# Kernel optimization log

Measured on AMD Instinct MI355X. Metric: run time of the kernel, lower is better.

The kernel has to match this reference:

```python
import jax, jax.numpy as jnp
import numpy as np

KERNEL_SIZE = 5
NUM_BUCKETS = 25


def setup_inputs() -> dict:
    key = jax.random.key(0)
    k1, k2, k3 = jax.random.split(key, 3)
    B, C, H, W = 8, 96, 192, 192
    inp = jax.random.normal(k1, (B, C, H, W), dtype=jnp.float32)
    kernel_bank = jax.random.normal(k2, (NUM_BUCKETS, KERNEL_SIZE, KERNEL_SIZE), dtype=jnp.float32)
    buckets = jax.random.randint(k3, (B, H, W), 0, NUM_BUCKETS, dtype=jnp.int64)
    return {"input": inp, "kernel_bank": kernel_bank, "buckets": buckets}


def reference(input, kernel_bank, buckets):
    # Per-pixel kernel selection from a bank, applied depthwise (same kernel for
    # every channel at a given spatial location), with 'same' zero padding.
    K = KERNEL_SIZE
    p = (K - 1) // 2
    B, C, H, W = input.shape
    xpad = jnp.pad(input, ((0, 0), (0, 0), (p, p), (p, p)))  # [B,C,H+K-1,W+K-1]
    kb = kernel_bank[buckets]  # [B,H,W,K,K] gathered per-pixel kernels
    out = jnp.zeros_like(input)
    # Fixed small loop over the K*K kernel taps (unrolled by jit); avoids
    # materializing a [B,C,H,W,K,K] patch tensor.
    for i in range(K):
        for j in range(K):
            out = out + xpad[:, :, i:i + H, j:j + W] * kb[:, None, :, :, i, j]
    return out
```

## Files before the change

### kernel.cpp

```cpp
#include <hip/hip_runtime.h>


#define KS 5
#define NB 25
#define HALO 2
#define TH 8
#define RPT 2
#define CPG 3
#define WID 192
#define HEI 192
#define CH 96
#define NBATCH 8
#define LPAD 4
#define LROW (LPAD + WID + LPAD)
#define LH (TH + 2 * HALO)
#define CSPLIT 4
#define CPB (CH / CSPLIT)
#define NTHREADS (WID * (TH / RPT))
#define HW ((size_t)HEI * WID)

static_assert(CPB % CPG == 0, "phase count integral");
static_assert(NTHREADS <= 1024, "block size limit");

__device__ __forceinline__ void async16(void* lds, const void* g) {
    __builtin_amdgcn_global_load_lds(
        (const __attribute__((address_space(1))) void*)g,
        (__attribute__((address_space(3))) void*)lds, 16, 0, 0);
}

#define WDECL(R)                                                              \
    float w##R##_0, w##R##_1, w##R##_2, w##R##_3, w##R##_4, w##R##_5,         \
        w##R##_6, w##R##_7, w##R##_8, w##R##_9, w##R##_10, w##R##_11,         \
        w##R##_12, w##R##_13, w##R##_14, w##R##_15, w##R##_16, w##R##_17,     \
        w##R##_18, w##R##_19, w##R##_20, w##R##_21, w##R##_22, w##R##_23,     \
        w##R##_24;

#define WGATH(R)                                                              \
    {                                                                         \
        const float* wp = &sb[bkt##R * (KS * KS)];                            \
        w##R##_0 = wp[0];   w##R##_1 = wp[1];   w##R##_2 = wp[2];             \
        w##R##_3 = wp[3];   w##R##_4 = wp[4];   w##R##_5 = wp[5];             \
        w##R##_6 = wp[6];   w##R##_7 = wp[7];   w##R##_8 = wp[8];             \
        w##R##_9 = wp[9];   w##R##_10 = wp[10]; w##R##_11 = wp[11];           \
        w##R##_12 = wp[12]; w##R##_13 = wp[13]; w##R##_14 = wp[14];           \
        w##R##_15 = wp[15]; w##R##_16 = wp[16]; w##R##_17 = wp[17];           \
        w##R##_18 = wp[18]; w##R##_19 = wp[19]; w##R##_20 = wp[20];           \
        w##R##_21 = wp[21]; w##R##_22 = wp[22]; w##R##_23 = wp[23];           \
        w##R##_24 = wp[24];                                                   \
    }

#define F5(R, T0, T1, T2, T3, T4)                                             \
    acc##R += x0 * w##R##_##T0 + x1 * w##R##_##T1 + x2 * w##R##_##T2          \
            + x3 * w##R##_##T3 + x4 * w##R##_##T4;

#define K0(R) F5(R, 0, 1, 2, 3, 4)
#define K1(R) F5(R, 5, 6, 7, 8, 9)
#define K2(R) F5(R, 10, 11, 12, 13, 14)
#define K3(R) F5(R, 15, 16, 17, 18, 19)
#define K4(R) F5(R, 20, 21, 22, 23, 24)

#define LOADX(CUR, SLAB, I)                                                   \
    {                                                                         \
        const float* rp = &sin_[CUR][SLAB][ty2 + (I)][wcol + (LPAD - HALO)];  \
        x0 = rp[0]; x1 = rp[1]; x2 = rp[2]; x3 = rp[3]; x4 = rp[4];           \
    }

__global__ __launch_bounds__(NTHREADS, 2) void csconv_kernel(
    const float* __restrict__ in, const float* __restrict__ bank,
    const int* __restrict__ buckets, float* __restrict__ out)
{
    __shared__ float sb[NB * KS * KS];
    __shared__ __align__(16) float sin_[2][CPG][LH][LROW];

    const int tid  = threadIdx.x;
    const int wcol = tid % WID;
    const int ty   = tid / WID;
    const int lane = tid & 63;
    const int wv   = tid >> 6;
    const int cg   = blockIdx.x;
    const int ht   = blockIdx.y;
    const int b    = blockIdx.z;
    const int h0   = ht * TH;
    const int r0   = h0 + ty * RPT;

    const int c0 = cg * CPB;
    const float* inb  = in  + (size_t)(b * CH + c0) * HW;
    float*       outb = out + (size_t)(b * CH + c0) * HW;

    if (tid < NB * KS * KS) sb[tid] = bank[tid];

    if (tid < 2 * CPG * LH * 8) {
        const int s = tid / (LH * 8), rem = tid % (LH * 8);
        const int r = rem / 8, p = rem % 8;
        const int col = (p < 4) ? p : (WID + p);
        sin_[s / CPG][s % CPG][r][col] = 0.0f;
    }
    if (h0 - HALO < 0) {
        for (int t = tid; t < 2 * CPG * 2 * LROW; t += NTHREADS) {
            const int s = t / (2 * LROW), rem = t % (2 * LROW);
            sin_[s / CPG][s % CPG][rem / LROW][rem % LROW] = 0.0f;
        }
    }
    if (h0 + TH + HALO > HEI) {
        for (int t = tid; t < 2 * CPG * 2 * LROW; t += NTHREADS) {
            const int s = t / (2 * LROW), rem = t % (2 * LROW);
            sin_[s / CPG][s % CPG][LH - 2 + rem / LROW][rem % LROW] = 0.0f;
        }
    }

#pragma unroll
    for (int k = 0; k < CPG; ++k) {
        const int m  = CPG * wv + k;
        const int s  = m / LH;
        const int rr = m % LH;
        const int hg = h0 - HALO + rr;
        if (hg >= 0 && hg < HEI && lane < 48)
            async16(&sin_[0][s][rr][LPAD],
                    inb + (size_t)s * HW + (size_t)hg * WID + lane * 4);
    }

    __syncthreads();

    const int bkt0 = buckets[(b * HEI + r0 + 0) * WID + wcol];
    const int bkt1 = buckets[(b * HEI + r0 + 1) * WID + wcol];
    WDECL(0) WDECL(1)
    WGATH(0) WGATH(1)

    const int ty2 = ty * RPT;

#define CONV_STORE(CUR, SLAB, CIDX)                                           \
    {                                                                         \
        float acc0 = 0.0f, acc1 = 0.0f;                                       \
        float x0, x1, x2, x3, x4;                                             \
        LOADX(CUR, SLAB, 0) K0(0)                                             \
        LOADX(CUR, SLAB, 1) K1(0) K0(1)                                       \
        LOADX(CUR, SLAB, 2) K2(0) K1(1)                                       \
        LOADX(CUR, SLAB, 3) K3(0) K2(1)                                       \
        LOADX(CUR, SLAB, 4) K4(0) K3(1)                                       \
        LOADX(CUR, SLAB, 5) K4(1)                                             \
        float* op = outb + (size_t)(CIDX) * HW + (size_t)r0 * WID + wcol;     \
        op[0 * WID] = acc0; op[1 * WID] = acc1;                               \
    }

    for (int c = 0; c < CPB; c += CPG) {
        const int cur = (c / CPG) & 1;
        const bool has_next = (c + CPG < CPB);

        if (has_next) {
            const int nxt = cur ^ 1;
#pragma unroll
            for (int k = 0; k < CPG; ++k) {
                const int m  = CPG * wv + k;
                const int s  = m / LH;
                const int rr = m % LH;
                const int hg = h0 - HALO + rr;
                if (hg >= 0 && hg < HEI && lane < 48)
                    async16(&sin_[nxt][s][rr][LPAD],
                            inb + (size_t)(c + CPG + s) * HW
                                + (size_t)hg * WID + lane * 4);
            }
        }

        CONV_STORE(cur, 0, c)
        CONV_STORE(cur, 1, c + 1)
        CONV_STORE(cur, 2, c + 2)

        if (has_next) {
            asm volatile("s_waitcnt vmcnt(6)" ::: "memory");
            __builtin_amdgcn_s_barrier();
            asm volatile("" ::: "memory");
        }
    }
}

extern "C" void kernel_launch(void* const* d_in, const int* in_sizes, int n_in,
                              void* d_out, int out_size, void* d_ws, size_t ws_size,
                              hipStream_t stream) {
    const float* in      = (const float*)d_in[0];
    const float* bank    = (const float*)d_in[1];
    const int*   buckets = (const int*)d_in[2];
    float*       out     = (float*)d_out;
    dim3 grid(CSPLIT, HEI / TH, NBATCH);
    csconv_kernel<<<grid, NTHREADS, 0, stream>>>(in, bank, buckets, out);
}
```

Measured before the change: 211.2 us.

## Tile width into 64-column blocks with halo loads and smaller channel groups

Splits the full 192-wide row tile into three 64-column tiles per block, each staging its own halo columns into LDS, and cuts the per-stage channel group from 3 to 2. Blocks shrink from 768 to 256 threads, the grid triples, and launch bounds now ask for 8 blocks per CU, aiming at higher occupancy and better latency hiding. The cost is redundant halo loads at tile edges and narrower, partly unaligned global-to-LDS copies.

```diff
diff --git a/kernel.cpp b/kernel.cpp
--- a/kernel.cpp
+++ b/kernel.cpp
@@ -6,21 +6,21 @@
 #define HALO 2
 #define TH 8
 #define RPT 2
-#define CPG 3
+#define CPG 2
+#define TILE 64
 #define WID 192
 #define HEI 192
 #define CH 96
 #define NBATCH 8
-#define LPAD 4
-#define LROW (LPAD + WID + LPAD)
+#define LROW (TILE + 8)
 #define LH (TH + 2 * HALO)
 #define CSPLIT 4
 #define CPB (CH / CSPLIT)
-#define NTHREADS (WID * (TH / RPT))
+#define NXT (WID / TILE)
+#define NTHREADS (TILE * (TH / RPT))
 #define HW ((size_t)HEI * WID)
 
 static_assert(CPB % CPG == 0, "phase count integral");
-static_assert(NTHREADS <= 1024, "block size limit");
 
 __device__ __forceinline__ void async16(void* lds, const void* g) {
     __builtin_amdgcn_global_load_lds(
@@ -61,72 +61,9 @@
 
 #define LOADX(CUR, SLAB, I)                                                   \
     {                                                                         \
-        const float* rp = &sin_[CUR][SLAB][ty2 + (I)][wcol + (LPAD - HALO)];  \
+        const float* rp = &sin_[CUR][SLAB][ty2 + (I)][xoff];                  \
         x0 = rp[0]; x1 = rp[1]; x2 = rp[2]; x3 = rp[3]; x4 = rp[4];           \
     }
-
-__global__ __launch_bounds__(NTHREADS, 2) void csconv_kernel(
-    const float* __restrict__ in, const float* __restrict__ bank,
-    const int* __restrict__ buckets, float* __restrict__ out)
-{
-    __shared__ float sb[NB * KS * KS];
-    __shared__ __align__(16) float sin_[2][CPG][LH][LROW];
-
-    const int tid  = threadIdx.x;
-    const int wcol = tid % WID;
-    const int ty   = tid / WID;
-    const int lane = tid & 63;
-    const int wv   = tid >> 6;
-    const int cg   = blockIdx.x;
-    const int ht   = blockIdx.y;
-    const int b    = blockIdx.z;
-    const int h0   = ht * TH;
-    const int r0   = h0 + ty * RPT;
-
-    const int c0 = cg * CPB;
-    const float* inb  = in  + (size_t)(b * CH + c0) * HW;
-    float*       outb = out + (size_t)(b * CH + c0) * HW;
-
-    if (tid < NB * KS * KS) sb[tid] = bank[tid];
-
-    if (tid < 2 * CPG * LH * 8) {
-        const int s = tid / (LH * 8), rem = tid % (LH * 8);
-        const int r = rem / 8, p = rem % 8;
-        const int col = (p < 4) ? p : (WID + p);
-        sin_[s / CPG][s % CPG][r][col] = 0.0f;
-    }
-    if (h0 - HALO < 0) {
-        for (int t = tid; t < 2 * CPG * 2 * LROW; t += NTHREADS) {
-            const int s = t / (2 * LROW), rem = t % (2 * LROW);
-            sin_[s / CPG][s % CPG][rem / LROW][rem % LROW] = 0.0f;
-        }
-    }
-    if (h0 + TH + HALO > HEI) {
-        for (int t = tid; t < 2 * CPG * 2 * LROW; t += NTHREADS) {
-            const int s = t / (2 * LROW), rem = t % (2 * LROW);
-            sin_[s / CPG][s % CPG][LH - 2 + rem / LROW][rem % LROW] = 0.0f;
-        }
-    }
-
-#pragma unroll
-    for (int k = 0; k < CPG; ++k) {
-        const int m  = CPG * wv + k;
-        const int s  = m / LH;
-        const int rr = m % LH;
-        const int hg = h0 - HALO + rr;
-        if (hg >= 0 && hg < HEI && lane < 48)
-            async16(&sin_[0][s][rr][LPAD],
-                    inb + (size_t)s * HW + (size_t)hg * WID + lane * 4);
-    }
-
-    __syncthreads();
-
-    const int bkt0 = buckets[(b * HEI + r0 + 0) * WID + wcol];
-    const int bkt1 = buckets[(b * HEI + r0 + 1) * WID + wcol];
-    WDECL(0) WDECL(1)
-    WGATH(0) WGATH(1)
-
-    const int ty2 = ty * RPT;
 
 #define CONV_STORE(CUR, SLAB, CIDX)                                           \
     {                                                                         \
@@ -138,35 +75,103 @@
         LOADX(CUR, SLAB, 3) K3(0) K2(1)                                       \
         LOADX(CUR, SLAB, 4) K4(0) K3(1)                                       \
         LOADX(CUR, SLAB, 5) K4(1)                                             \
-        float* op = outb + (size_t)(CIDX) * HW + (size_t)r0 * WID + wcol;     \
-        op[0 * WID] = acc0; op[1 * WID] = acc1;                               \
+        float* op = outb + (size_t)(CIDX) * HW + (size_t)r0 * WID + gcol;     \
+        op[0] = acc0; op[WID] = acc1;                                         \
     }
+
+#define STAGE(BUF, CBASE)                                                     \
+    _Pragma("unroll")                                                         \
+    for (int k = 0; k < 6; ++k) {                                             \
+        const int m  = 6 * wv + k;                                 \
+        const int s  = m / LH;                                 \
+        const int rr = m % LH;                          \
+        const int hg = h0 - HALO + rr;                                        \
+        if (hg >= 0 && hg < HEI && lane < nl)                                 \
+            async16(&sin_[BUF][s][rr][dst0],                                  \
+                    inb + (size_t)((CBASE) + s) * HW + (size_t)hg * WID       \
+                        + src0 + lane * 4);                                   \
+    }
+
+__global__ __launch_bounds__(NTHREADS, 8) void csconv_kernel(
+    const float* __restrict__ in, const float* __restrict__ bank,
+    const int* __restrict__ buckets, float* __restrict__ out)
+{
+    __shared__ float sb[NB * KS * KS];
+    __shared__ __align__(16) float sin_[2][CPG][LH][LROW];
+
+    const int tid  = threadIdx.x;
+    const int wcol = tid % TILE;
+    const int ty   = tid / TILE;
+    const int lane = tid & 63;
+    const int wv   = tid >> 6;
+    const int bx   = blockIdx.x;
+    const int cx   = bx % NXT;
+    const int cg   = bx / NXT;
+    const int ht   = blockIdx.y;
+    const int b    = blockIdx.z;
+    const int h0   = ht * TH;
+    const int r0   = h0 + ty * RPT;
+    const int gcol = cx * TILE + wcol;
+
+    const int c0 = cg * CPB;
+    const float* inb  = in  + (size_t)(b * CH + c0) * HW;
+    float*       outb = out + (size_t)(b * CH + c0) * HW;
+
+    const int src0 = (cx == 0) ? 0 : (cx * TILE - 4);
+    const int dst0 = (cx == 0) ? 4 : 0;
+    const int nl   = (cx == 1) ? 18 : 17;
+
+    for (int t = tid; t < NB * KS * KS; t += NTHREADS) sb[t] = bank[t];
+
+    if (cx != 1 && tid < 2 * CPG * LH * 4) {
+        const int buf = tid / (CPG * LH * 4);
+        const int s   = (tid / (LH * 4)) % CPG;
+        const int r   = (tid / 4) % LH;
+        const int p   = tid & 3;
+        sin_[buf][s][r][(cx == 0 ? 0 : TILE + 4) + p] = 0.0f;
+    }
+    if (h0 - HALO < 0) {
+        for (int t = tid; t < 2 * CPG * 2 * LROW; t += NTHREADS) {
+            const int buf = t / (CPG * 2 * LROW);
+            const int rem = t % (CPG * 2 * LROW);
+            const int s   = rem / (2 * LROW);
+            const int r   = (rem / LROW) % 2;
+            sin_[buf][s][r][rem % LROW] = 0.0f;
+        }
+    }
+    if (h0 + TH + HALO > HEI) {
+        for (int t = tid; t < 2 * CPG * 2 * LROW; t += NTHREADS) {
+            const int buf = t / (CPG * 2 * LROW);
+            const int rem = t % (CPG * 2 * LROW);
+            const int s   = rem / (2 * LROW);
+            const int r   = (rem / LROW) % 2;
+            sin_[buf][s][LH - 2 + r][rem % LROW] = 0.0f;
+        }
+    }
+
+    STAGE(0, 0)
+
+    __syncthreads();
+
+    const int bkt0 = buckets[(b * HEI + r0 + 0) * WID + gcol];
+    const int bkt1 = buckets[(b * HEI + r0 + 1) * WID + gcol];
+    WDECL(0) WDECL(1)
+    WGATH(0) WGATH(1)
+
+    const int ty2  = ty * RPT;
+    const int xoff = wcol + 2;
 
     for (int c = 0; c < CPB; c += CPG) {
         const int cur = (c / CPG) & 1;
         const bool has_next = (c + CPG < CPB);
 
-        if (has_next) {
-            const int nxt = cur ^ 1;
-#pragma unroll
-            for (int k = 0; k < CPG; ++k) {
-                const int m  = CPG * wv + k;
-                const int s  = m / LH;
-                const int rr = m % LH;
-                const int hg = h0 - HALO + rr;
-                if (hg >= 0 && hg < HEI && lane < 48)
-                    async16(&sin_[nxt][s][rr][LPAD],
-                            inb + (size_t)(c + CPG + s) * HW
-                                + (size_t)hg * WID + lane * 4);
-            }
-        }
+        if (has_next) STAGE(cur ^ 1, c + CPG)
 
         CONV_STORE(cur, 0, c)
         CONV_STORE(cur, 1, c + 1)
-        CONV_STORE(cur, 2, c + 2)
 
         if (has_next) {
-            asm volatile("s_waitcnt vmcnt(6)" ::: "memory");
+            asm volatile("s_waitcnt vmcnt(4)" ::: "memory");
             __builtin_amdgcn_s_barrier();
             asm volatile("" ::: "memory");
         }
@@ -180,6 +185,6 @@
     const float* bank    = (const float*)d_in[1];
     const int*   buckets = (const int*)d_in[2];
     float*       out     = (float*)d_out;
-    dim3 grid(CSPLIT, HEI / TH, NBATCH);
+    dim3 grid(NXT * CSPLIT, HEI / TH, NBATCH);
     csconv_kernel<<<grid, NTHREADS, 0, stream>>>(in, bank, buckets, out);
 }
```

After: 462.2 us. +118.8%, slower.
